# Optimization experiments

Hardware: AMD Instinct MI355X
Metric: run time of the kernel (lower is better)

## Reference

```python
import jax, jax.numpy as jnp
import numpy as np
import math

E = 1024   # embedding_size
H = 16     # layer_size (num heads)
DK = 64    # key_size
DH = 64    # head_size
HID = 4096 # hidden_size
B = 2
S = 2048   # context_size
EPS = 1e-5


def layer_norm(x, w, b):
    mu = jnp.mean(x, axis=-1, keepdims=True)
    var = jnp.mean(jnp.square(x - mu), axis=-1, keepdims=True)
    return (x - mu) * jax.lax.rsqrt(var + EPS) * w + b


def setup_inputs() -> dict:
    key = jax.random.key(0)
    ks = jax.random.split(key, 16)
    sE = 1.0 / math.sqrt(E)
    sH = 1.0 / math.sqrt(HID)
    return {
        "embeddings": jax.random.normal(ks[0], (B, S, E), dtype=jnp.float32),
        "Wq": jax.random.uniform(ks[1], (H, E, DK), minval=-sE, maxval=sE, dtype=jnp.float32),
        "bq": jnp.zeros((H, DK), dtype=jnp.float32),
        "Wk": jax.random.uniform(ks[2], (H, E, DK), minval=-sE, maxval=sE, dtype=jnp.float32),
        "bk": jnp.zeros((H, DK), dtype=jnp.float32),
        "Wv": jax.random.uniform(ks[3], (H, E, DH), minval=-sE, maxval=sE, dtype=jnp.float32),
        "bv": jnp.zeros((H, DH), dtype=jnp.float32),
        "ln1_w": jnp.ones((E,), dtype=jnp.float32),
        "ln1_b": jnp.zeros((E,), dtype=jnp.float32),
        "ln2_w": jnp.ones((E,), dtype=jnp.float32),
        "ln2_b": jnp.zeros((E,), dtype=jnp.float32),
        "W1": jax.random.uniform(ks[4], (E, HID), minval=-sE, maxval=sE, dtype=jnp.float32),
        "b1": jnp.zeros((HID,), dtype=jnp.float32),
        "W2": jax.random.uniform(ks[5], (HID, E), minval=-sH, maxval=sH, dtype=jnp.float32),
        "b2": jnp.zeros((E,), dtype=jnp.float32),
    }


def reference(embeddings, Wq, bq, Wk, bk, Wv, bv, ln1_w, ln1_b, ln2_w, ln2_b, W1, b1, W2, b2):
    # NOTE: faithful to source: residual uses the POST-norm activations
    # (embeddings is reassigned to the LayerNorm output before the residual add).
    x = layer_norm(embeddings, ln1_w, ln1_b)            # [B,S,E]
    q = jnp.einsum('bse,hed->bhsd', x, Wq) + bq[:, None, :]
    k = jnp.einsum('bse,hed->bhsd', x, Wk) + bk[:, None, :]
    v = jnp.einsum('bse,hed->bhsd', x, Wv) + bv[:, None, :]
    scores = jnp.einsum('bhsd,bhtd->bhst', q, k) / math.sqrt(DK)  # [B,H,S,S]
    causal = jnp.tril(jnp.ones((S, S), dtype=bool))
    scores = jnp.where(causal, scores, -jnp.inf)
    w = jax.nn.softmax(scores, axis=-1)
    o = jnp.einsum('bhst,bhtd->bhsd', w, v)             # [B,H,S,DH]
    o = jnp.transpose(o, (0, 2, 1, 3)).reshape(B, S, H * DH)  # concat heads
    x = x + o
    y = layer_norm(x, ln2_w, ln2_b)
    h = jax.nn.relu(jnp.einsum('bse,eh->bsh', y, W1) + b1)
    out = y + jnp.einsum('bsh,he->bse', h, W2) + b2
    return out
```

## Files before the change

kernel.cpp:

```cpp
#include <hip/hip_runtime.h>


typedef unsigned short u16;
typedef unsigned int   u32;
typedef __bf16 bf16x8 __attribute__((ext_vector_type(8)));
typedef float  f32x4  __attribute__((ext_vector_type(4)));

#define NEG_INF (-__builtin_inff())

#if __has_builtin(__builtin_amdgcn_exp2f)
#define EXP2F(x) __builtin_amdgcn_exp2f(x)
#else
#define EXP2F(x) exp2f(x)
#endif

struct PartPtrs { float* h[6]; };

__device__ __forceinline__ u32 pack_bf16_trunc(float a, float b) {
#if __has_builtin(__builtin_amdgcn_perm)
  return __builtin_amdgcn_perm(__float_as_uint(b), __float_as_uint(a), 0x07060302u);
#else
  return (__float_as_uint(a) >> 16) | (__float_as_uint(b) & 0xFFFF0000u);
#endif
}

__device__ __forceinline__ u16 f2b(float f) {
  u32 u = __float_as_uint(f);
  u = (u + 0x7fffu + ((u >> 16) & 1u)) >> 16;
  return (u16)u;
}

__device__ __forceinline__ void gload16(const void* g, void* l) {
  __builtin_amdgcn_global_load_lds(
      (const __attribute__((address_space(1))) u32*)g,
      (__attribute__((address_space(3))) u32*)l, 16, 0, 0);
}

__device__ __forceinline__ bf16x8 ld16(const u16* p) { return *(const bf16x8*)p; }

__global__ __launch_bounds__(256)
void transpose_qkv_k(const float* __restrict__ Wq, const float* __restrict__ Wk,
                     const float* __restrict__ Wv, u16* __restrict__ out) {
  __shared__ float tile[64][65];
  int z = blockIdx.z, which = z >> 4, sub = z & 15;
  const float* in = which == 0 ? Wq : (which == 1 ? Wk : Wv);
  const float* ip = in + (size_t)sub * 1024 * 64;
  u16* op = out + (size_t)which * 1024 * 1024 + (size_t)sub * 64 * 1024;
  int r0 = blockIdx.x * 64;
  int tr = threadIdx.x >> 6, tc = threadIdx.x & 63;
#pragma unroll
  for (int i = 0; i < 16; i++) {
    int r = i * 4 + tr;
    tile[r][tc] = ip[(size_t)(r0 + r) * 64 + tc];
  }
  __syncthreads();
#pragma unroll
  for (int i = 0; i < 16; i++) {
    int c = i * 4 + tr;
    op[(size_t)c * 1024 + r0 + tc] = f2b(tile[tc][c]);
  }
}

__global__ __launch_bounds__(256)
void transpose_w12_k(const float* __restrict__ W1, const float* __restrict__ W2,
                     u16* __restrict__ W1t, u16* __restrict__ W2t) {
  __shared__ float tile[64][65];
  int id = blockIdx.x;
  const float* in; u16* out; int R, C, r0, c0;
  if (id < 1024) { in = W1; out = W1t; R = 1024; C = 4096; r0 = (id & 15) * 64; c0 = (id >> 4) * 64; }
  else { id -= 1024; in = W2; out = W2t; R = 4096; C = 1024; r0 = (id >> 4) * 64; c0 = (id & 15) * 64; }
  int tr = threadIdx.x >> 6, tc = threadIdx.x & 63;
#pragma unroll
  for (int i = 0; i < 16; i++) {
    int r = i * 4 + tr;
    tile[r][tc] = in[(size_t)(r0 + r) * C + c0 + tc];
  }
  __syncthreads();
#pragma unroll
  for (int i = 0; i < 16; i++) {
    int c = i * 4 + tr;
    out[(size_t)(c0 + c) * R + r0 + tc] = f2b(tile[tc][c]);
  }
}

__global__ __launch_bounds__(256)
void vtrans_k(const u16* __restrict__ vin, u16* __restrict__ vt) {
  __shared__ __align__(16) u16 tile[64][72];
  int s0 = blockIdx.x * 64, bh = blockIdx.y;
  const u16* ip = vin + (size_t)bh * 2048 * 64;
  u16* op = vt + (size_t)bh * 64 * 2048;
  int t = threadIdx.x;
#pragma unroll
  for (int i = 0; i < 2; i++) {
    int idx = i * 256 + t, r = idx >> 3, c = idx & 7;
    *(uint4*)&tile[r][c * 8] = *(const uint4*)(ip + (size_t)(s0 + r) * 64 + c * 8);
  }
  __syncthreads();
#pragma unroll
  for (int i = 0; i < 16; i++) {
    int d = i * 4 + (t >> 6), s = t & 63;
    op[(size_t)d * 2048 + s0 + s] = tile[s][d];
  }
}

__global__ __launch_bounds__(256)
void ln_k(const float* __restrict__ in, const float* __restrict__ in2,
          const float* __restrict__ w, const float* __restrict__ b,
          float* __restrict__ outf, u16* __restrict__ outb) {
  int row = blockIdx.x, t = threadIdx.x;
  const float4* ip = (const float4*)(in + (size_t)row * 1024);
  float4 x = ip[t];
  if (in2) {
    const float4* ip2 = (const float4*)(in2 + (size_t)row * 1024);
    float4 o = ip2[t];
    x.x += o.x; x.y += o.y; x.z += o.z; x.w += o.w;
  }
  float s = x.x + x.y + x.z + x.w;
  float q = x.x * x.x + x.y * x.y + x.z * x.z + x.w * x.w;
#pragma unroll
  for (int m = 32; m; m >>= 1) { s += __shfl_xor(s, m); q += __shfl_xor(q, m); }
  __shared__ float rs[4], rq[4];
  if ((t & 63) == 0) { rs[t >> 6] = s; rq[t >> 6] = q; }
  __syncthreads();
  s = rs[0] + rs[1] + rs[2] + rs[3];
  q = rq[0] + rq[1] + rq[2] + rq[3];
  float mean = s * (1.f / 1024.f);
  float var  = q * (1.f / 1024.f) - mean * mean;
  float rstd = rsqrtf(var + 1e-5f);
  float4 wv = ((const float4*)w)[t];
  float4 bv = ((const float4*)b)[t];
  float4 y;
  y.x = (x.x - mean) * rstd * wv.x + bv.x;
  y.y = (x.y - mean) * rstd * wv.y + bv.y;
  y.z = (x.z - mean) * rstd * wv.z + bv.z;
  y.w = (x.w - mean) * rstd * wv.w + bv.w;
  if (outf) ((float4*)(outf + (size_t)row * 1024))[t] = y;
  ushort4 ub;
  ub.x = f2b(y.x); ub.y = f2b(y.y); ub.z = f2b(y.z); ub.w = f2b(y.w);
  ((ushort4*)(outb + (size_t)row * 1024))[t] = ub;
}

#define EPI_QKV  0
#define EPI_RELU 1
#define EPI_RES  2

#define QSCALE 0.18033688011112042f

template <int EPI>
__device__ __forceinline__
void gemm_body(const u16* __restrict__ A, const u16* __restrict__ Bt,
               int K, int lda, int ldbt,
               const float* __restrict__ bias0, const float* __restrict__ bias1,
               const float* __restrict__ bias2, const float* __restrict__ res,
               int ldout, u16* __restrict__ outb, float* __restrict__ outf,
               float* __restrict__ outp) {
  __shared__ __align__(16) u16 As[128 * 64];
  __shared__ __align__(16) u16 Bs[128 * 64];
  int t = threadIdx.x;
  int wave = t >> 6, lane = t & 63, quad = lane >> 4, l16 = lane & 15;
  int x7 = l16 & 7;
  int wm = (wave >> 1) * 64, wn = (wave & 1) * 64;
  int bm = blockIdx.x * 128, bn = blockIdx.y * 128;
  int zoff = blockIdx.z * K;

  const u16* Agl[4];
  const u16* Bgl[4];
#pragma unroll
  for (int i = 0; i < 4; i++) {
    int idx = i * 256 + t, r = idx >> 3, c = (idx & 7) ^ (r & 7);
    Agl[i] = A + (size_t)(bm + r) * lda + zoff + c * 8;
    Bgl[i] = Bt + (size_t)(bn + r) * ldbt + zoff + c * 8;
  }
  u16* Asl = As + t * 8;
  u16* Bsl = Bs + t * 8;

  f32x4 acc[4][4] = {};

  for (int k0 = 0; k0 < K; k0 += 64) {
#pragma unroll
    for (int i = 0; i < 4; i++) {
      gload16(Agl[i] + k0, Asl + i * 2048);
      gload16(Bgl[i] + k0, Bsl + i * 2048);
    }
    __syncthreads();
#pragma unroll
    for (int kc = 0; kc < 2; kc++) {
      bf16x8 af[4], bfr[4];
#pragma unroll
      for (int i = 0; i < 4; i++) {
        int r = wm + i * 16 + l16;
        af[i] = *(const bf16x8*)(As + r * 64 + (((kc * 4 + quad) ^ x7) * 8));
      }
#pragma unroll
      for (int j = 0; j < 4; j++) {
        int r = wn + j * 16 + l16;
        bfr[j] = *(const bf16x8*)(Bs + r * 64 + (((kc * 4 + quad) ^ x7) * 8));
      }
#pragma unroll
      for (int i = 0; i < 4; i++)
#pragma unroll
        for (int j = 0; j < 4; j++)
          acc[i][j] = __builtin_amdgcn_mfma_f32_16x16x32_bf16(af[i], bfr[j],
                                                              acc[i][j], 0, 0, 0);
    }
    __syncthreads();
  }

#pragma unroll
  for (int i = 0; i < 4; i++) {
#pragma unroll
    for (int j = 0; j < 4; j++) {
      int c = bn + wn + j * 16 + l16;
#pragma unroll
      for (int rr = 0; rr < 4; rr++) {
        int r = bm + wm + i * 16 + quad * 4 + rr;
        float v = acc[i][j][rr];
        if (EPI == EPI_QKV) {
          int which = c >> 10, h = (c >> 6) & 15, d = c & 63;
          const float* bp = which == 0 ? bias0 : (which == 1 ? bias1 : bias2);
          v += bp[h * 64 + d];
          if (which == 0) v *= QSCALE;
          int bb = r >> 11, ss = r & 2047;
          outb[((size_t)(which * 32 + bb * 16 + h) * 2048 + ss) * 64 + d] = f2b(v);
        } else if (EPI == EPI_RELU) {
          v += bias0[c];
          v = v > 0.f ? v : 0.f;
          outb[(size_t)r * ldout + c] = f2b(v);
        } else {
          if (blockIdx.z == 0) {
            v += bias0[c] + res[(size_t)r * ldout + c];
            outf[(size_t)r * ldout + c] = v;
          } else {
            outp[(size_t)(r & 2047) * ldout + c] = v;
          }
        }
      }
    }
  }
}

__global__ __launch_bounds__(256)
void qkv_gemm(const u16* A, const u16* Bt, int K, int lda, int ldbt,
              const float* b0, const float* b1, const float* b2,
              u16* outb) {
  gemm_body<EPI_QKV>(A, Bt, K, lda, ldbt, b0, b1, b2, nullptr, 0, outb, nullptr, nullptr);
}
__global__ __launch_bounds__(256)
void ffn1_gemm(const u16* A, const u16* Bt, int K, int lda, int ldbt,
               const float* b0, int ldout, u16* outb) {
  gemm_body<EPI_RELU>(A, Bt, K, lda, ldbt, b0, nullptr, nullptr, nullptr, ldout, outb, nullptr, nullptr);
}
__global__ __launch_bounds__(256)
void ffn2_gemm(const u16* A, const u16* Bt, int K, int lda, int ldbt,
               const float* b0, const float* res, int ldout,
               float* outf, PartPtrs parts) {
  float* pp = nullptr;
  if (blockIdx.z) pp = parts.h[(blockIdx.z - 1) * 2 + (blockIdx.x >> 4)];
  gemm_body<EPI_RES>(A, Bt, K, lda, ldbt, b0, nullptr, nullptr, res, ldout,
                     nullptr, outf, pp);
}

__global__ __launch_bounds__(256)
void reduce_k(float* __restrict__ out, PartPtrs parts) {
  int i = blockIdx.x * 256 + threadIdx.x;
  int half = i >> 19;
  int off  = i & ((1 << 19) - 1);
  float4 b = ((float4*)out)[i];
#pragma unroll
  for (int z = 0; z < 3; z++) {
    float4 a = ((const float4*)parts.h[z * 2 + half])[off];
    b.x += a.x; b.y += a.y; b.z += a.z; b.w += a.w;
  }
  ((float4*)out)[i] = b;
}

__global__ __launch_bounds__(512, 6)
void attn_k(const u16* __restrict__ qkv, const u16* __restrict__ vt,
            float* __restrict__ o) {
  int bh = blockIdx.y, b = bh >> 4, h = bh & 15;
  int Qt = b ? (15 - (int)blockIdx.x) : (int)blockIdx.x;
  int t = threadIdx.x;
  int wave = t >> 6, lane = t & 63, quad = lane >> 4, l16 = lane & 15;
  int x7 = l16 & 7;
  int q0 = Qt * 128 + wave * 16;

  const u16* qg = qkv + (size_t)bh * (2048 * 64);
  const u16* kg = qkv + (size_t)(32 + bh) * (2048 * 64);
  const u16* vg = vt + (size_t)bh * (64 * 2048);

  __shared__ __align__(16) u16 Ks[2][64 * 64];
  __shared__ __align__(16) u16 Vs[2][64 * 64];
  __shared__ __align__(16) u16 Ps[8][16 * 64 + 32];
  u16* Pw = Ps[wave];
  float* auxf = (float*)(Pw + 1024);

  int sr = t >> 3, sc_ = (t & 7) ^ (sr & 7);

  gload16(kg + (size_t)sr * 64 + sc_ * 8, Ks[0] + t * 8);
  gload16(vg + (size_t)sr * 2048 + sc_ * 8, Vs[0] + t * 8);

  bf16x8 qf0 = ld16(qg + (size_t)(q0 + l16) * 64 + quad * 8);
  bf16x8 qf1 = ld16(qg + (size_t)(q0 + l16) * 64 + 32 + quad * 8);

  f32x4 oacc[4] = {};
  float mo = NEG_INF, ll = 0.f;
  int kmax_w = q0 >> 6;
  int klast = 2 * Qt + 1;

  __syncthreads();

  for (int kt = 0; kt <= klast; kt++) {
    const u16* ks = Ks[kt & 1];
    const u16* vs = Vs[kt & 1];
    if (kt < klast) {
      gload16(kg + (size_t)((kt + 1) * 64 + sr) * 64 + sc_ * 8, Ks[(kt + 1) & 1] + t * 8);
      gload16(vg + (size_t)sr * 2048 + (kt + 1) * 64 + sc_ * 8, Vs[(kt + 1) & 1] + t * 8);
    }
    if (kt <= kmax_w) {
      f32x4 sc[4];
#pragma unroll
      for (int g = 0; g < 4; g++) {
        const u16* kr = ks + (g * 16 + l16) * 64;
        bf16x8 kf0 = *(const bf16x8*)(kr + ((quad ^ x7) * 8));
        bf16x8 kf1 = *(const bf16x8*)(kr + (((4 + quad) ^ x7) * 8));
        f32x4 s = {};
        s = __builtin_amdgcn_mfma_f32_16x16x32_bf16(kf0, qf0, s, 0, 0, 0);
        s = __builtin_amdgcn_mfma_f32_16x16x32_bf16(kf1, qf1, s, 0, 0, 0);
        sc[g] = s;
      }

      if (kt == kmax_w) {
#pragma unroll
        for (int g = 0; g < 4; g++) {
          int kvb = kt * 64 + g * 16 + quad * 4;
#pragma unroll
          for (int rr = 0; rr < 4; rr++)
            if (kvb + rr > q0 + l16) sc[g][rr] = NEG_INF;
        }
      }

      float mx = sc[0][0];
#pragma unroll
      for (int g = 0; g < 4; g++)
#pragma unroll
        for (int rr = 0; rr < 4; rr++) mx = fmaxf(mx, sc[g][rr]);
      mx = fmaxf(mx, __shfl_xor(mx, 16));
      mx = fmaxf(mx, __shfl_xor(mx, 32));
      float mnew = fmaxf(mo, mx);
      float al = EXP2F(mo - mnew);
      mo = mnew;

      float sum = 0.f;
#pragma unroll
      for (int g = 0; g < 4; g++) {
        float p0 = EXP2F(sc[g][0] - mnew);
        float p1 = EXP2F(sc[g][1] - mnew);
        float p2 = EXP2F(sc[g][2] - mnew);
        float p3 = EXP2F(sc[g][3] - mnew);
        sum += (p0 + p1) + (p2 + p3);
        u32 lo = pack_bf16_trunc(p0, p1);
        u32 hi = pack_bf16_trunc(p2, p3);
        int slot = (2 * g + (quad >> 1)) ^ x7;
        *(uint2*)(Pw + l16 * 64 + slot * 8 + (quad & 1) * 4) = make_uint2(lo, hi);
      }
      sum += __shfl_xor(sum, 16);
      sum += __shfl_xor(sum, 32);
      ll = ll * al + sum;

      if (lane < 16) auxf[lane] = al;
      f32x4 av = *(const f32x4*)(auxf + quad * 4);
#pragma unroll
      for (int g = 0; g < 4; g++)
#pragma unroll
        for (int rr = 0; rr < 4; rr++) oacc[g][rr] *= av[rr];

      bf16x8 pf0 = *(const bf16x8*)(Pw + l16 * 64 + ((quad ^ x7) * 8));
      bf16x8 pf1 = *(const bf16x8*)(Pw + l16 * 64 + (((4 + quad) ^ x7) * 8));
#pragma unroll
      for (int g = 0; g < 4; g++) {
        const u16* vr = vs + (g * 16 + l16) * 64;
        bf16x8 vf0 = *(const bf16x8*)(vr + ((quad ^ x7) * 8));
        bf16x8 vf1 = *(const bf16x8*)(vr + (((4 + quad) ^ x7) * 8));
        oacc[g] = __builtin_amdgcn_mfma_f32_16x16x32_bf16(pf0, vf0, oacc[g], 0, 0, 0);
        oacc[g] = __builtin_amdgcn_mfma_f32_16x16x32_bf16(pf1, vf1, oacc[g], 0, 0, 0);
      }
    }
    __syncthreads();
  }

  if (lane < 16) auxf[lane] = ll;
  f32x4 lv = *(const f32x4*)(auxf + quad * 4);
  float rinv[4];
#pragma unroll
  for (int rr = 0; rr < 4; rr++) rinv[rr] = 1.f / lv[rr];
  float* op = o + ((size_t)b * 2048 + q0) * 1024 + h * 64;
#pragma unroll
  for (int g = 0; g < 4; g++)
#pragma unroll
    for (int rr = 0; rr < 4; rr++)
      op[(size_t)(quad * 4 + rr) * 1024 + g * 16 + l16] = oacc[g][rr] * rinv[rr];
}

extern "C" void kernel_launch(void* const* d_in, const int* in_sizes, int n_in,
                              void* d_out, int out_size, void* d_ws, size_t ws_size,
                              hipStream_t stream) {
  const float* emb  = (const float*)d_in[0];
  const float* Wq   = (const float*)d_in[1];
  const float* bq   = (const float*)d_in[2];
  const float* Wk   = (const float*)d_in[3];
  const float* bk   = (const float*)d_in[4];
  const float* Wv   = (const float*)d_in[5];
  const float* bv   = (const float*)d_in[6];
  const float* ln1w = (const float*)d_in[7];
  const float* ln1b = (const float*)d_in[8];
  const float* ln2w = (const float*)d_in[9];
  const float* ln2b = (const float*)d_in[10];
  const float* W1   = (const float*)d_in[11];
  const float* b1   = (const float*)d_in[12];
  const float* W2   = (const float*)d_in[13];
  const float* b2   = (const float*)d_in[14];
  float* out = (float*)d_out;

  char* p = (char*)d_ws;
  u16*   Wqkv_t = (u16*)p;   p += (size_t)3072 * 1024 * 2;
  u16*   W1t    = (u16*)p;   p += (size_t)4096 * 1024 * 2;
  u16*   W2t    = (u16*)p;   p += (size_t)1024 * 4096 * 2;
  float* x      = (float*)p; p += (size_t)4096 * 1024 * 4;
  u16*   xb     = (u16*)p;   p += (size_t)4096 * 1024 * 2;
  u16*   qkvb   = (u16*)p;   p += (size_t)3 * 32 * 2048 * 64 * 2;
  float* ob     = (float*)p; p += (size_t)4096 * 1024 * 4;
  float* y      = (float*)p; p += (size_t)4096 * 1024 * 4;
  u16*   yb     = (u16*)p;   p += (size_t)4096 * 1024 * 2;
  u16*   hb     = (u16*)qkvb;
  u16*   vT     = (u16*)y;
  if (ws_size < (size_t)(p - (char*)d_ws)) return;

  PartPtrs parts;
  parts.h[0] = x;
  parts.h[1] = x + (size_t)2048 * 1024;
  parts.h[2] = (float*)xb;
  parts.h[3] = (float*)((char*)ob + (size_t)2048 * 1024 * 4);
  parts.h[4] = (float*)W1t;
  parts.h[5] = (float*)yb;

  transpose_qkv_k<<<dim3(16, 1, 48), 256, 0, stream>>>(Wq, Wk, Wv, Wqkv_t);
  transpose_w12_k<<<dim3(2048), 256, 0, stream>>>(W1, W2, W1t, W2t);

  ln_k<<<dim3(4096), 256, 0, stream>>>(emb, nullptr, ln1w, ln1b, x, xb);

  qkv_gemm<<<dim3(32, 24, 1), 256, 0, stream>>>(
      xb, Wqkv_t, 1024, 1024, 1024, bq, bk, bv, qkvb);

  vtrans_k<<<dim3(32, 32), 256, 0, stream>>>(qkvb + (size_t)64 * 2048 * 64, vT);

  attn_k<<<dim3(16, 32), 512, 0, stream>>>(qkvb, vT, ob);

  ln_k<<<dim3(4096), 256, 0, stream>>>(x, ob, ln2w, ln2b, y, yb);

  ffn1_gemm<<<dim3(32, 32, 1), 256, 0, stream>>>(
      yb, W1t, 1024, 1024, 1024, b1, 4096, hb);

  ffn2_gemm<<<dim3(32, 8, 4), 256, 0, stream>>>(
      hb, W2t, 1024, 4096, 4096, b2, y, 1024, out, parts);

  reduce_k<<<dim3(4096), 256, 0, stream>>>(out, parts);
}
```

Baseline: 348.5 us.

## Rewrite GEMMs as 256x256 double-buffered tiles with interleaved loads and MFMA

```diff
diff --git a/kernel.cpp b/kernel.cpp
--- a/kernel.cpp
+++ b/kernel.cpp
@@ -37,6 +37,9 @@
 }
 
 __device__ __forceinline__ bf16x8 ld16(const u16* p) { return *(const bf16x8*)p; }
+
+#define SCHED0() __builtin_amdgcn_sched_barrier(0)
+#define SBAR()   __builtin_amdgcn_s_barrier()
 
 __global__ __launch_bounds__(256)
 void transpose_qkv_k(const float* __restrict__ Wq, const float* __restrict__ Wk,
@@ -148,72 +151,111 @@
 
 template <int EPI>
 __device__ __forceinline__
-void gemm_body(const u16* __restrict__ A, const u16* __restrict__ Bt,
-               int K, int lda, int ldbt,
-               const float* __restrict__ bias0, const float* __restrict__ bias1,
-               const float* __restrict__ bias2, const float* __restrict__ res,
-               int ldout, u16* __restrict__ outb, float* __restrict__ outf,
-               float* __restrict__ outp) {
-  __shared__ __align__(16) u16 As[128 * 64];
-  __shared__ __align__(16) u16 Bs[128 * 64];
+void gemm256_body(const u16* __restrict__ A, const u16* __restrict__ Bt,
+                  int K, int lda, int ldbt,
+                  const float* __restrict__ bias0, const float* __restrict__ bias1,
+                  const float* __restrict__ bias2, const float* __restrict__ res,
+                  int ldout, u16* __restrict__ outb, float* __restrict__ outf,
+                  float* __restrict__ outp) {
+  __shared__ __align__(16) u16 As[2][256 * 64];
+  __shared__ __align__(16) u16 Bs[2][256 * 64];
   int t = threadIdx.x;
   int wave = t >> 6, lane = t & 63, quad = lane >> 4, l16 = lane & 15;
   int x7 = l16 & 7;
-  int wm = (wave >> 1) * 64, wn = (wave & 1) * 64;
-  int bm = blockIdx.x * 128, bn = blockIdx.y * 128;
+  int wr0 = (wave >> 2) * 128, wc0 = (wave & 3) * 64;
+  int bm = blockIdx.x * 256, bn = blockIdx.y * 256;
   int zoff = blockIdx.z * K;
 
-  const u16* Agl[4];
-  const u16* Bgl[4];
+  const u16* Ag[4];
+  const u16* Bg[4];
 #pragma unroll
   for (int i = 0; i < 4; i++) {
-    int idx = i * 256 + t, r = idx >> 3, c = (idx & 7) ^ (r & 7);
-    Agl[i] = A + (size_t)(bm + r) * lda + zoff + c * 8;
-    Bgl[i] = Bt + (size_t)(bn + r) * ldbt + zoff + c * 8;
-  }
-  u16* Asl = As + t * 8;
-  u16* Bsl = Bs + t * 8;
-
-  f32x4 acc[4][4] = {};
-
-  for (int k0 = 0; k0 < K; k0 += 64) {
-#pragma unroll
-    for (int i = 0; i < 4; i++) {
-      gload16(Agl[i] + k0, Asl + i * 2048);
-      gload16(Bgl[i] + k0, Bsl + i * 2048);
+    int idx = i * 512 + t, r = idx >> 3, c = (idx & 7) ^ (r & 7);
+    Ag[i] = A + (size_t)(bm + r) * lda + zoff + c * 8;
+    Bg[i] = Bt + (size_t)(bn + r) * ldbt + zoff + c * 8;
+  }
+
+  f32x4 acc[8][4] = {};
+
+  int nk = K >> 6;
+  {
+    u16* Ad = (u16*)As[0] + t * 8;
+    u16* Bd = (u16*)Bs[0] + t * 8;
+    gload16(Bg[0], Bd);
+    gload16(Bg[1], Bd + 4096);
+    gload16(Bg[2], Bd + 2 * 4096);
+    gload16(Bg[3], Bd + 3 * 4096);
+    gload16(Ag[0], Ad);
+    gload16(Ag[2], Ad + 2 * 4096);
+    gload16(Ag[1], Ad + 4096);
+    gload16(Ag[3], Ad + 3 * 4096);
+  }
+  asm volatile("s_waitcnt vmcnt(2)" ::: "memory");
+  SCHED0();
+  SBAR();
+  SCHED0();
+
+  for (int kt = 0; kt < nk; kt++) {
+    int b = kt & 1;
+    const u16* Ab = As[b];
+    const u16* Bb = Bs[b];
+    int hn = (kt + 1 < nk);
+    int ko = (kt + 1) << 6;
+    u16* Ad = (u16*)As[b ^ 1] + t * 8;
+    u16* Bd = (u16*)Bs[b ^ 1] + t * 8;
+
+#pragma unroll
+    for (int ph = 0; ph < 4; ph++) {
+      const int kc = ph & 1, mh = ph >> 1;
+      bf16x8 af[4], bfr[4];
+#pragma unroll
+      for (int i = 0; i < 4; i++) {
+        int r = wr0 + (mh * 4 + i) * 16 + l16;
+        af[i] = *(const bf16x8*)(Ab + r * 64 + (((kc * 4 + quad) ^ x7) * 8));
+      }
+#pragma unroll
+      for (int j = 0; j < 4; j++) {
+        int r = wc0 + j * 16 + l16;
+        bfr[j] = *(const bf16x8*)(Bb + r * 64 + (((kc * 4 + quad) ^ x7) * 8));
+      }
+      if (hn) {
+        if (ph == 0)      { gload16(Bg[0] + ko, Bd);            gload16(Bg[1] + ko, Bd + 4096); }
+        else if (ph == 1) { gload16(Bg[2] + ko, Bd + 2 * 4096); gload16(Bg[3] + ko, Bd + 3 * 4096); }
+        else if (ph == 2) { gload16(Ag[0] + ko, Ad);            gload16(Ag[2] + ko, Ad + 2 * 4096); }
+        else              { gload16(Ag[1] + ko, Ad + 4096);     gload16(Ag[3] + ko, Ad + 3 * 4096); }
+      }
+      SCHED0();
+      SBAR();
+      SCHED0();
+      __builtin_amdgcn_s_setprio(1);
+#pragma unroll
+      for (int i = 0; i < 4; i++)
+#pragma unroll
+        for (int j = 0; j < 4; j++)
+          acc[mh * 4 + i][j] = __builtin_amdgcn_mfma_f32_16x16x32_bf16(
+              af[i], bfr[j], acc[mh * 4 + i][j], 0, 0, 0);
+      __builtin_amdgcn_s_setprio(0);
+      SCHED0();
+      if (ph == 1) {
+        if (hn) asm volatile("s_waitcnt vmcnt(4)" ::: "memory");
+        else    asm volatile("s_waitcnt vmcnt(0)" ::: "memory");
+        SCHED0();
+      } else if (ph == 3) {
+        if (hn) { asm volatile("s_waitcnt vmcnt(2)" ::: "memory"); SCHED0(); }
+      }
+      SBAR();
+      SCHED0();
     }
-    __syncthreads();
-#pragma unroll
-    for (int kc = 0; kc < 2; kc++) {
-      bf16x8 af[4], bfr[4];
-#pragma unroll
-      for (int i = 0; i < 4; i++) {
-        int r = wm + i * 16 + l16;
-        af[i] = *(const bf16x8*)(As + r * 64 + (((kc * 4 + quad) ^ x7) * 8));
-      }
-#pragma unroll
-      for (int j = 0; j < 4; j++) {
-        int r = wn + j * 16 + l16;
-        bfr[j] = *(const bf16x8*)(Bs + r * 64 + (((kc * 4 + quad) ^ x7) * 8));
-      }
-#pragma unroll
-      for (int i = 0; i < 4; i++)
-#pragma unroll
-        for (int j = 0; j < 4; j++)
-          acc[i][j] = __builtin_amdgcn_mfma_f32_16x16x32_bf16(af[i], bfr[j],
-                                                              acc[i][j], 0, 0, 0);
-    }
-    __syncthreads();
-  }
-
-#pragma unroll
-  for (int i = 0; i < 4; i++) {
+  }
+
+#pragma unroll
+  for (int i = 0; i < 8; i++) {
 #pragma unroll
     for (int j = 0; j < 4; j++) {
-      int c = bn + wn + j * 16 + l16;
+      int c = bn + wc0 + j * 16 + l16;
 #pragma unroll
       for (int rr = 0; rr < 4; rr++) {
-        int r = bm + wm + i * 16 + quad * 4 + rr;
+        int r = bm + wr0 + i * 16 + quad * 4 + rr;
         float v = acc[i][j][rr];
         if (EPI == EPI_QKV) {
           int which = c >> 10, h = (c >> 6) & 15, d = c & 63;
@@ -239,25 +281,29 @@
   }
 }
 
-__global__ __launch_bounds__(256)
+__global__ __launch_bounds__(512, 2)
 void qkv_gemm(const u16* A, const u16* Bt, int K, int lda, int ldbt,
               const float* b0, const float* b1, const float* b2,
               u16* outb) {
-  gemm_body<EPI_QKV>(A, Bt, K, lda, ldbt, b0, b1, b2, nullptr, 0, outb, nullptr, nullptr);
-}
-__global__ __launch_bounds__(256)
+  gemm256_body<EPI_QKV>(A, Bt, K, lda, ldbt, b0, b1, b2, nullptr, 0, outb,
+                        nullptr, nullptr);
+}
+
+__global__ __launch_bounds__(512, 2)
 void ffn1_gemm(const u16* A, const u16* Bt, int K, int lda, int ldbt,
                const float* b0, int ldout, u16* outb) {
-  gemm_body<EPI_RELU>(A, Bt, K, lda, ldbt, b0, nullptr, nullptr, nullptr, ldout, outb, nullptr, nullptr);
-}
-__global__ __launch_bounds__(256)
+  gemm256_body<EPI_RELU>(A, Bt, K, lda, ldbt, b0, nullptr, nullptr, nullptr,
+                         ldout, outb, nullptr, nullptr);
+}
+
+__global__ __launch_bounds__(512, 2)
 void ffn2_gemm(const u16* A, const u16* Bt, int K, int lda, int ldbt,
                const float* b0, const float* res, int ldout,
                float* outf, PartPtrs parts) {
   float* pp = nullptr;
-  if (blockIdx.z) pp = parts.h[(blockIdx.z - 1) * 2 + (blockIdx.x >> 4)];
-  gemm_body<EPI_RES>(A, Bt, K, lda, ldbt, b0, nullptr, nullptr, res, ldout,
-                     nullptr, outf, pp);
+  if (blockIdx.z) pp = parts.h[(blockIdx.z - 1) * 2 + (blockIdx.x >> 3)];
+  gemm256_body<EPI_RES>(A, Bt, K, lda, ldbt, b0, nullptr, nullptr, res, ldout,
+                        nullptr, outf, pp);
 }
 
 __global__ __launch_bounds__(256)
@@ -448,7 +494,7 @@
 
   ln_k<<<dim3(4096), 256, 0, stream>>>(emb, nullptr, ln1w, ln1b, x, xb);
 
-  qkv_gemm<<<dim3(32, 24, 1), 256, 0, stream>>>(
+  qkv_gemm<<<dim3(16, 12, 1), 512, 0, stream>>>(
       xb, Wqkv_t, 1024, 1024, 1024, bq, bk, bv, qkvb);
 
   vtrans_k<<<dim3(32, 32), 256, 0, stream>>>(qkvb + (size_t)64 * 2048 * 64, vT);
@@ -457,10 +503,10 @@
 
   ln_k<<<dim3(4096), 256, 0, stream>>>(x, ob, ln2w, ln2b, y, yb);
 
-  ffn1_gemm<<<dim3(32, 32, 1), 256, 0, stream>>>(
+  ffn1_gemm<<<dim3(16, 16, 1), 512, 0, stream>>>(
       yb, W1t, 1024, 1024, 1024, b1, 4096, hb);
 
-  ffn2_gemm<<<dim3(32, 8, 4), 256, 0, stream>>>(
+  ffn2_gemm<<<dim3(16, 4, 4), 512, 0, stream>>>(
       hb, W2t, 1024, 4096, 4096, b2, y, 1024, out, parts);
 
   reduce_k<<<dim3(4096), 256, 0, stream>>>(out, parts);
```

Measured after the change: 347.2 us. About the same (-0.4%).
